# Performance work log

Measured on AMD Instinct MI355X. Metric: run time of the kernel, lower is better.

Reference implementation:

```python
import jax, jax.numpy as jnp
import numpy as np

# Topologies derived from init kwargs (inputs=64, outputs=64, state=512, net1 hidden=[512])
D = 64 + 64 + 512                      # 640 = concat(input, prev_output, state)
NET1 = [D, 512, 64]
NET3 = [D] + NET1 + [512]              # [640, 640, 512, 64, 512] (code reuses mutated net1 topo)
W_TOTAL = sum(NET3[j] * NET3[j + 1] for j in range(len(NET3) - 1))  # 802816
B_TOTAL = sum(NET3[1:])                # 1728
NET2 = [D] + NET1 + [W_TOTAL + B_TOTAL]  # [640, 640, 512, 64, 804544]


def _leaky(v):
    return jnp.where(v >= 0, v, 0.01 * v)


def setup_inputs() -> dict:
    key = jax.random.key(0)
    ks = jax.random.split(key, 16)
    inp = {
        "x": jax.random.normal(ks[0], (64,), jnp.float32),
        "prev_output": jnp.zeros((64,), jnp.float32),
        "state": jnp.zeros((512,), jnp.float32),
    }
    # net1 params (Linear stores W as [out, in])
    for i in range(len(NET1) - 1):
        inp[f"net1_w{i}"] = jax.random.normal(ks[1 + i], (NET1[i + 1], NET1[i]), jnp.float32) * 0.02
        inp[f"net1_b{i}"] = jnp.zeros((NET1[i + 1],), jnp.float32)
    # net2 params
    for i in range(len(NET2) - 1):
        inp[f"net2_w{i}"] = jax.random.normal(ks[5 + i], (NET2[i + 1], NET2[i]), jnp.float32) * 0.02
        inp[f"net2_b{i}"] = jnp.zeros((NET2[i + 1],), jnp.float32)
    return inp


def reference(x, prev_output, state,
              net1_w0, net1_b0, net1_w1, net1_b1,
              net2_w0, net2_b0, net2_w1, net2_b1,
              net2_w2, net2_b2, net2_w3, net2_b3):
    inpt = jnp.concatenate([x, prev_output, state])  # [640]

    # net2: hypernetwork producing flattened weights+biases for net3
    h = _leaky(net2_w0 @ inpt + net2_b0)
    h = _leaky(net2_w1 @ h + net2_b1)
    h = _leaky(net2_w2 @ h + net2_b2)
    x2 = jnp.tanh(net2_w3 @ h + net2_b3) * 0.5       # [W_TOTAL + B_TOTAL]
    weights = x2[:W_TOTAL]
    bias = x2[W_TOTAL:]

    # net3: apply generated weights sequentially (state update)
    x3 = inpt
    wi, bi = 0, 0
    for j in range(1, len(NET3)):
        out_d, in_d = NET3[j], NET3[j - 1]
        W = weights[wi:wi + out_d * in_d].reshape(out_d, in_d)
        b = bias[bi:bi + out_d]
        x3 = W @ x3 + b                               # 1D: x3 @ W.T == W @ x3
        if j != len(NET3) - 1:
            x3 = _leaky(x3)
        wi += out_d * in_d
        bi += out_d
    new_state = x3                                    # [512]

    # net1: output head
    h1 = _leaky(net1_w0 @ inpt + net1_b0)
    out = net1_w1 @ h1 + net1_b1                      # [64]

    # torch forward returns only `out`; new_state is the persistent buffer
    # update. We concatenate both so the full step math is observable.
    return jnp.concatenate([out, new_state])          # [576]
```

## Files before the change

### kernel.cpp

```cpp
#include <hip/hip_runtime.h>
#include <math.h>


#define WS_H0    0
#define WS_H1N1  640
#define WS_H1N2  1152
#define WS_H2    1664
#define WS_INPT  1728
#define WS_X3A   2368
#define WS_X3B   3008
#define WS_X3C   3520

__device__ __forceinline__ float leaky_f(float v) { return v >= 0.0f ? v : 0.01f * v; }

__device__ __forceinline__ float inpt_at(int i, const float* x, const float* po, const float* st) {
  return i < 64 ? x[i] : (i < 128 ? po[i - 64] : st[i - 128]);
}

__global__ __launch_bounds__(256) void k1a(const float* __restrict__ x, const float* __restrict__ po,
                                           const float* __restrict__ st,
                                           const float* __restrict__ w2_0, const float* __restrict__ b2_0,
                                           const float* __restrict__ w1_0, const float* __restrict__ b1_0,
                                           float* __restrict__ ws) {
  __shared__ float s_in[640];
  for (int i = threadIdx.x; i < 640; i += 256) {
    float v = inpt_at(i, x, po, st);
    s_in[i] = v;
    ws[WS_INPT + i] = v;
  }
  __syncthreads();
  int wave = threadIdx.x >> 6, lane = threadIdx.x & 63;
  int o = blockIdx.x * 4 + wave;
  const float* wrow;
  float bias;
  float* dst;
  if (o < 640) {
    wrow = w2_0 + (long long)o * 640; bias = b2_0[o]; dst = ws + WS_H0 + o;
  } else {
    int oo = o - 640;
    wrow = w1_0 + (long long)oo * 640; bias = b1_0[oo]; dst = ws + WS_H1N1 + oo;
  }
  float acc = 0.0f;
  for (int i = lane; i < 640; i += 64) acc += wrow[i] * s_in[i];
  for (int off = 32; off; off >>= 1) acc += __shfl_xor(acc, off, 64);
  if (lane == 0) *dst = leaky_f(acc + bias);
}

__global__ __launch_bounds__(256) void k1b(const float* __restrict__ w2_1, const float* __restrict__ b2_1,
                                           const float* __restrict__ w1_1, const float* __restrict__ b1_1,
                                           float* __restrict__ ws, float* __restrict__ out) {
  __shared__ float s_h0[640];
  __shared__ float s_h1[512];
  for (int i = threadIdx.x; i < 640; i += 256) s_h0[i] = ws[WS_H0 + i];
  for (int i = threadIdx.x; i < 512; i += 256) s_h1[i] = ws[WS_H1N1 + i];
  __syncthreads();
  int wave = threadIdx.x >> 6, lane = threadIdx.x & 63;
  int o = blockIdx.x * 4 + wave;
  float acc = 0.0f;
  if (o < 512) {
    const float* wrow = w2_1 + (long long)o * 640;
    for (int i = lane; i < 640; i += 64) acc += wrow[i] * s_h0[i];
    for (int off = 32; off; off >>= 1) acc += __shfl_xor(acc, off, 64);
    if (lane == 0) ws[WS_H1N2 + o] = leaky_f(acc + b2_1[o]);
  } else {
    int oo = o - 512;
    const float* wrow = w1_1 + (long long)oo * 512;
    for (int i = lane; i < 512; i += 64) acc += wrow[i] * s_h1[i];
    for (int off = 32; off; off >>= 1) acc += __shfl_xor(acc, off, 64);
    if (lane == 0) out[oo] = acc + b1_1[oo];
  }
}

__global__ __launch_bounds__(256) void k1c(const float* __restrict__ w2_2, const float* __restrict__ b2_2,
                                           float* __restrict__ ws) {
  __shared__ float s_h[512];
  for (int i = threadIdx.x; i < 512; i += 256) s_h[i] = ws[WS_H1N2 + i];
  __syncthreads();
  int wave = threadIdx.x >> 6, lane = threadIdx.x & 63;
  int o = blockIdx.x * 4 + wave;
  const float* wrow = w2_2 + (long long)o * 512;
  float acc = 0.0f;
  for (int i = lane; i < 512; i += 64) acc += wrow[i] * s_h[i];
  for (int off = 32; off; off >>= 1) acc += __shfl_xor(acc, off, 64);
  if (lane == 0) ws[WS_H2 + o] = leaky_f(acc + b2_2[o]);
}

template <int IN_D, bool LEAKY>
__global__ __launch_bounds__(256) void k2(const float* __restrict__ w3, const float* __restrict__ b3,
                                          const float* __restrict__ h2p, const float* __restrict__ x3in,
                                          float* __restrict__ x3out, long long wi, long long brow) {
  __shared__ float s_in[IN_D];
  __shared__ float s_red[4];
  float h[64];
  const float4* h4 = (const float4*)h2p;
#pragma unroll
  for (int k = 0; k < 16; k++) {
    float4 v = h4[k];
    h[4 * k + 0] = v.x; h[4 * k + 1] = v.y; h[4 * k + 2] = v.z; h[4 * k + 3] = v.w;
  }
  for (int i = threadIdx.x; i < IN_D; i += 256) s_in[i] = x3in[i];
  __syncthreads();

  int o = blockIdx.x;
  float acc = 0.0f;
  for (int i = threadIdx.x; i < IN_D; i += 256) {
    long long r = wi + (long long)o * IN_D + i;
    const float4* row = (const float4*)(w3 + r * 64);
    float d = 0.0f;
#pragma unroll
    for (int k = 0; k < 16; k++) {
      float4 v = row[k];
      d += v.x * h[4 * k + 0] + v.y * h[4 * k + 1] + v.z * h[4 * k + 2] + v.w * h[4 * k + 3];
    }
    float x2v = 0.5f * tanhf(d + b3[r]);
    acc += x2v * s_in[i];
  }
  for (int off = 32; off; off >>= 1) acc += __shfl_xor(acc, off, 64);
  int wave = threadIdx.x >> 6, lane = threadIdx.x & 63;
  if (lane == 0) s_red[wave] = acc;
  __syncthreads();
  if (threadIdx.x == 0) {
    float tot = s_red[0] + s_red[1] + s_red[2] + s_red[3];
    long long rb = brow + o;
    const float4* row = (const float4*)(w3 + rb * 64);
    float d = 0.0f;
#pragma unroll
    for (int k = 0; k < 16; k++) {
      float4 v = row[k];
      d += v.x * h[4 * k + 0] + v.y * h[4 * k + 1] + v.z * h[4 * k + 2] + v.w * h[4 * k + 3];
    }
    float gb = 0.5f * tanhf(d + b3[rb]);
    float res = tot + gb;
    x3out[o] = LEAKY ? leaky_f(res) : res;
  }
}

__global__ __launch_bounds__(256) void k2d(const float* __restrict__ w3, const float* __restrict__ b3,
                                           const float* __restrict__ ws, float* __restrict__ out) {
  const float* h2p = ws + WS_H2;
  float h[64];
  const float4* h4 = (const float4*)h2p;
#pragma unroll
  for (int k = 0; k < 16; k++) {
    float4 v = h4[k];
    h[4 * k + 0] = v.x; h[4 * k + 1] = v.y; h[4 * k + 2] = v.z; h[4 * k + 3] = v.w;
  }
  int wave = threadIdx.x >> 6, lane = threadIdx.x & 63;
  int o = blockIdx.x * 4 + wave;
  long long r = 770048LL + (long long)o * 64 + lane;
  const float4* row = (const float4*)(w3 + r * 64);
  float d = 0.0f;
#pragma unroll
  for (int k = 0; k < 16; k++) {
    float4 v = row[k];
    d += v.x * h[4 * k + 0] + v.y * h[4 * k + 1] + v.z * h[4 * k + 2] + v.w * h[4 * k + 3];
  }
  float x2v = 0.5f * tanhf(d + b3[r]);
  float acc = x2v * ws[WS_X3C + lane];
  for (int off = 32; off; off >>= 1) acc += __shfl_xor(acc, off, 64);
  if (lane == 0) {
    long long rb = 804032LL + o;
    const float4* brow = (const float4*)(w3 + rb * 64);
    float db = 0.0f;
#pragma unroll
    for (int k = 0; k < 16; k++) {
      float4 v = brow[k];
      db += v.x * h[4 * k + 0] + v.y * h[4 * k + 1] + v.z * h[4 * k + 2] + v.w * h[4 * k + 3];
    }
    float gb = 0.5f * tanhf(db + b3[rb]);
    out[64 + o] = acc + gb;
  }
}

extern "C" void kernel_launch(void* const* d_in, const int* in_sizes, int n_in,
                              void* d_out, int out_size, void* d_ws, size_t ws_size,
                              hipStream_t stream) {
  const float* x    = (const float*)d_in[0];
  const float* po   = (const float*)d_in[1];
  const float* st   = (const float*)d_in[2];
  const float* w1_0 = (const float*)d_in[3];
  const float* b1_0 = (const float*)d_in[4];
  const float* w1_1 = (const float*)d_in[5];
  const float* b1_1 = (const float*)d_in[6];
  const float* w2_0 = (const float*)d_in[7];
  const float* b2_0 = (const float*)d_in[8];
  const float* w2_1 = (const float*)d_in[9];
  const float* b2_1 = (const float*)d_in[10];
  const float* w2_2 = (const float*)d_in[11];
  const float* b2_2 = (const float*)d_in[12];
  const float* w3   = (const float*)d_in[13];
  const float* b3   = (const float*)d_in[14];
  float* ws  = (float*)d_ws;
  float* out = (float*)d_out;

  k1a<<<288, 256, 0, stream>>>(x, po, st, w2_0, b2_0, w1_0, b1_0, ws);
  k1b<<<144, 256, 0, stream>>>(w2_1, b2_1, w1_1, b1_1, ws, out);
  k1c<<<16, 256, 0, stream>>>(w2_2, b2_2, ws);
  k2<640, true><<<640, 256, 0, stream>>>(w3, b3, ws + WS_H2, ws + WS_INPT, ws + WS_X3A, 0LL, 802816LL);
  k2<640, true><<<512, 256, 0, stream>>>(w3, b3, ws + WS_H2, ws + WS_X3A, ws + WS_X3B, 409600LL, 803456LL);
  k2<512, true><<<64, 256, 0, stream>>>(w3, b3, ws + WS_H2, ws + WS_X3B, ws + WS_X3C, 737280LL, 803968LL);
  k2d<<<128, 256, 0, stream>>>(w3, b3, ws, out);
}
```

Before: 354.8 us.

## Vectorize dot products, uniform hidden vector, fast tanh, and 512-thread blocks for generator

Several changes land together. The net1/net2 row dot products now use float4 loads from global and shared memory. The generator kernels read the 64-element hidden vector through readfirstlane so it can live in scalar registers, and compute tanh with exp2 and a hardware reciprocal instead of tanhf. The generated-bias row is folded into the per-thread work rather than computed serially by thread 0. The k2 launches also move to 512 threads per block. The intent is to cut VGPR pressure and transcendental cost in a memory-bound kernel. The fast tanh approximation may change accuracy slightly, and with 512 threads a block for the 640-input layers has only 128 threads doing a second iteration, so load imbalance grows.

```diff
diff --git a/kernel.cpp b/kernel.cpp
--- a/kernel.cpp
+++ b/kernel.cpp
@@ -13,8 +13,55 @@
 
 __device__ __forceinline__ float leaky_f(float v) { return v >= 0.0f ? v : 0.01f * v; }
 
+__device__ __forceinline__ float uni(float v) {
+  return __int_as_float(__builtin_amdgcn_readfirstlane(__float_as_int(v)));
+}
+
 __device__ __forceinline__ float inpt_at(int i, const float* x, const float* po, const float* st) {
   return i < 64 ? x[i] : (i < 128 ? po[i - 64] : st[i - 128]);
+}
+
+__device__ __forceinline__ float x2val(const float* __restrict__ w3, const float* __restrict__ b3,
+                                       long long r, const float* hs) {
+  const float4* row = (const float4*)(w3 + (r << 6));
+  float d0 = 0.f, d1 = 0.f, d2 = 0.f, d3 = 0.f;
+#pragma unroll
+  for (int k = 0; k < 16; k++) {
+    float4 v = row[k];
+    d0 = fmaf(v.x, hs[4 * k + 0], d0);
+    d1 = fmaf(v.y, hs[4 * k + 1], d1);
+    d2 = fmaf(v.z, hs[4 * k + 2], d2);
+    d3 = fmaf(v.w, hs[4 * k + 3], d3);
+  }
+  float d = ((d0 + d1) + (d2 + d3)) + b3[r];
+  float t = exp2f(d * 2.8853900817779268f);
+  return 0.5f - __builtin_amdgcn_rcpf(t + 1.0f);
+}
+
+__device__ __forceinline__ void load_h_uniform(const float* __restrict__ h2p, float* hs) {
+  const float4* h4 = (const float4*)h2p;
+#pragma unroll
+  for (int k = 0; k < 16; k++) {
+    float4 v = h4[k];
+    hs[4 * k + 0] = uni(v.x);
+    hs[4 * k + 1] = uni(v.y);
+    hs[4 * k + 2] = uni(v.z);
+    hs[4 * k + 3] = uni(v.w);
+  }
+}
+
+template <int IN>
+__device__ __forceinline__ float row_dot(const float* __restrict__ wrow, const float* s_in, int lane) {
+  const float4* w4 = (const float4*)wrow;
+  const float4* s4 = (const float4*)s_in;
+  float acc = 0.f;
+  for (int j = lane; j < IN / 4; j += 64) {
+    float4 a = w4[j];
+    float4 b = s4[j];
+    acc += a.x * b.x + a.y * b.y + a.z * b.z + a.w * b.w;
+  }
+  for (int off = 32; off; off >>= 1) acc += __shfl_xor(acc, off, 64);
+  return acc;
 }
 
 __global__ __launch_bounds__(256) void k1a(const float* __restrict__ x, const float* __restrict__ po,
@@ -22,7 +69,7 @@
                                            const float* __restrict__ w2_0, const float* __restrict__ b2_0,
                                            const float* __restrict__ w1_0, const float* __restrict__ b1_0,
                                            float* __restrict__ ws) {
-  __shared__ float s_in[640];
+  __shared__ __align__(16) float s_in[640];
   for (int i = threadIdx.x; i < 640; i += 256) {
     float v = inpt_at(i, x, po, st);
     s_in[i] = v;
@@ -40,136 +87,83 @@
     int oo = o - 640;
     wrow = w1_0 + (long long)oo * 640; bias = b1_0[oo]; dst = ws + WS_H1N1 + oo;
   }
-  float acc = 0.0f;
-  for (int i = lane; i < 640; i += 64) acc += wrow[i] * s_in[i];
-  for (int off = 32; off; off >>= 1) acc += __shfl_xor(acc, off, 64);
+  float acc = row_dot<640>(wrow, s_in, lane);
   if (lane == 0) *dst = leaky_f(acc + bias);
 }
 
 __global__ __launch_bounds__(256) void k1b(const float* __restrict__ w2_1, const float* __restrict__ b2_1,
                                            const float* __restrict__ w1_1, const float* __restrict__ b1_1,
                                            float* __restrict__ ws, float* __restrict__ out) {
-  __shared__ float s_h0[640];
-  __shared__ float s_h1[512];
+  __shared__ __align__(16) float s_h0[640];
+  __shared__ __align__(16) float s_h1[512];
   for (int i = threadIdx.x; i < 640; i += 256) s_h0[i] = ws[WS_H0 + i];
   for (int i = threadIdx.x; i < 512; i += 256) s_h1[i] = ws[WS_H1N1 + i];
   __syncthreads();
   int wave = threadIdx.x >> 6, lane = threadIdx.x & 63;
   int o = blockIdx.x * 4 + wave;
-  float acc = 0.0f;
   if (o < 512) {
-    const float* wrow = w2_1 + (long long)o * 640;
-    for (int i = lane; i < 640; i += 64) acc += wrow[i] * s_h0[i];
-    for (int off = 32; off; off >>= 1) acc += __shfl_xor(acc, off, 64);
+    float acc = row_dot<640>(w2_1 + (long long)o * 640, s_h0, lane);
     if (lane == 0) ws[WS_H1N2 + o] = leaky_f(acc + b2_1[o]);
   } else {
     int oo = o - 512;
-    const float* wrow = w1_1 + (long long)oo * 512;
-    for (int i = lane; i < 512; i += 64) acc += wrow[i] * s_h1[i];
-    for (int off = 32; off; off >>= 1) acc += __shfl_xor(acc, off, 64);
+    float acc = row_dot<512>(w1_1 + (long long)oo * 512, s_h1, lane);
     if (lane == 0) out[oo] = acc + b1_1[oo];
   }
 }
 
 __global__ __launch_bounds__(256) void k1c(const float* __restrict__ w2_2, const float* __restrict__ b2_2,
                                            float* __restrict__ ws) {
-  __shared__ float s_h[512];
+  __shared__ __align__(16) float s_h[512];
   for (int i = threadIdx.x; i < 512; i += 256) s_h[i] = ws[WS_H1N2 + i];
   __syncthreads();
   int wave = threadIdx.x >> 6, lane = threadIdx.x & 63;
   int o = blockIdx.x * 4 + wave;
-  const float* wrow = w2_2 + (long long)o * 512;
-  float acc = 0.0f;
-  for (int i = lane; i < 512; i += 64) acc += wrow[i] * s_h[i];
-  for (int off = 32; off; off >>= 1) acc += __shfl_xor(acc, off, 64);
+  float acc = row_dot<512>(w2_2 + (long long)o * 512, s_h, lane);
   if (lane == 0) ws[WS_H2 + o] = leaky_f(acc + b2_2[o]);
 }
 
 template <int IN_D, bool LEAKY>
-__global__ __launch_bounds__(256) void k2(const float* __restrict__ w3, const float* __restrict__ b3,
+__global__ __launch_bounds__(512) void k2(const float* __restrict__ w3, const float* __restrict__ b3,
                                           const float* __restrict__ h2p, const float* __restrict__ x3in,
                                           float* __restrict__ x3out, long long wi, long long brow) {
-  __shared__ float s_in[IN_D];
-  __shared__ float s_red[4];
-  float h[64];
-  const float4* h4 = (const float4*)h2p;
-#pragma unroll
-  for (int k = 0; k < 16; k++) {
-    float4 v = h4[k];
-    h[4 * k + 0] = v.x; h[4 * k + 1] = v.y; h[4 * k + 2] = v.z; h[4 * k + 3] = v.w;
-  }
-  for (int i = threadIdx.x; i < IN_D; i += 256) s_in[i] = x3in[i];
+  __shared__ __align__(16) float s_in[IN_D];
+  __shared__ float s_red[8];
+  float hs[64];
+  load_h_uniform(h2p, hs);
+  for (int i = threadIdx.x; i < IN_D; i += 512) s_in[i] = x3in[i];
   __syncthreads();
 
   int o = blockIdx.x;
   float acc = 0.0f;
-  for (int i = threadIdx.x; i < IN_D; i += 256) {
+  for (int i = threadIdx.x; i < IN_D; i += 512) {
     long long r = wi + (long long)o * IN_D + i;
-    const float4* row = (const float4*)(w3 + r * 64);
-    float d = 0.0f;
-#pragma unroll
-    for (int k = 0; k < 16; k++) {
-      float4 v = row[k];
-      d += v.x * h[4 * k + 0] + v.y * h[4 * k + 1] + v.z * h[4 * k + 2] + v.w * h[4 * k + 3];
-    }
-    float x2v = 0.5f * tanhf(d + b3[r]);
-    acc += x2v * s_in[i];
+    acc += x2val(w3, b3, r, hs) * s_in[i];
   }
+  if (threadIdx.x == 511) acc += x2val(w3, b3, brow + o, hs);
+
   for (int off = 32; off; off >>= 1) acc += __shfl_xor(acc, off, 64);
   int wave = threadIdx.x >> 6, lane = threadIdx.x & 63;
   if (lane == 0) s_red[wave] = acc;
   __syncthreads();
   if (threadIdx.x == 0) {
-    float tot = s_red[0] + s_red[1] + s_red[2] + s_red[3];
-    long long rb = brow + o;
-    const float4* row = (const float4*)(w3 + rb * 64);
-    float d = 0.0f;
+    float tot = 0.f;
 #pragma unroll
-    for (int k = 0; k < 16; k++) {
-      float4 v = row[k];
-      d += v.x * h[4 * k + 0] + v.y * h[4 * k + 1] + v.z * h[4 * k + 2] + v.w * h[4 * k + 3];
-    }
-    float gb = 0.5f * tanhf(d + b3[rb]);
-    float res = tot + gb;
-    x3out[o] = LEAKY ? leaky_f(res) : res;
+    for (int w = 0; w < 8; w++) tot += s_red[w];
+    x3out[o] = LEAKY ? leaky_f(tot) : tot;
   }
 }
 
 __global__ __launch_bounds__(256) void k2d(const float* __restrict__ w3, const float* __restrict__ b3,
                                            const float* __restrict__ ws, float* __restrict__ out) {
-  const float* h2p = ws + WS_H2;
-  float h[64];
-  const float4* h4 = (const float4*)h2p;
-#pragma unroll
-  for (int k = 0; k < 16; k++) {
-    float4 v = h4[k];
-    h[4 * k + 0] = v.x; h[4 * k + 1] = v.y; h[4 * k + 2] = v.z; h[4 * k + 3] = v.w;
-  }
+  float hs[64];
+  load_h_uniform(ws + WS_H2, hs);
   int wave = threadIdx.x >> 6, lane = threadIdx.x & 63;
   int o = blockIdx.x * 4 + wave;
   long long r = 770048LL + (long long)o * 64 + lane;
-  const float4* row = (const float4*)(w3 + r * 64);
-  float d = 0.0f;
-#pragma unroll
-  for (int k = 0; k < 16; k++) {
-    float4 v = row[k];
-    d += v.x * h[4 * k + 0] + v.y * h[4 * k + 1] + v.z * h[4 * k + 2] + v.w * h[4 * k + 3];
-  }
-  float x2v = 0.5f * tanhf(d + b3[r]);
-  float acc = x2v * ws[WS_X3C + lane];
+  float acc = x2val(w3, b3, r, hs) * ws[WS_X3C + lane];
+  if (lane == 0) acc += x2val(w3, b3, 804032LL + o, hs);
   for (int off = 32; off; off >>= 1) acc += __shfl_xor(acc, off, 64);
-  if (lane == 0) {
-    long long rb = 804032LL + o;
-    const float4* brow = (const float4*)(w3 + rb * 64);
-    float db = 0.0f;
-#pragma unroll
-    for (int k = 0; k < 16; k++) {
-      float4 v = brow[k];
-      db += v.x * h[4 * k + 0] + v.y * h[4 * k + 1] + v.z * h[4 * k + 2] + v.w * h[4 * k + 3];
-    }
-    float gb = 0.5f * tanhf(db + b3[rb]);
-    out[64 + o] = acc + gb;
-  }
+  if (lane == 0) out[64 + o] = acc;
 }
 
 extern "C" void kernel_launch(void* const* d_in, const int* in_sizes, int n_in,
@@ -196,8 +190,8 @@
   k1a<<<288, 256, 0, stream>>>(x, po, st, w2_0, b2_0, w1_0, b1_0, ws);
   k1b<<<144, 256, 0, stream>>>(w2_1, b2_1, w1_1, b1_1, ws, out);
   k1c<<<16, 256, 0, stream>>>(w2_2, b2_2, ws);
-  k2<640, true><<<640, 256, 0, stream>>>(w3, b3, ws + WS_H2, ws + WS_INPT, ws + WS_X3A, 0LL, 802816LL);
-  k2<640, true><<<512, 256, 0, stream>>>(w3, b3, ws + WS_H2, ws + WS_X3A, ws + WS_X3B, 409600LL, 803456LL);
-  k2<512, true><<<64, 256, 0, stream>>>(w3, b3, ws + WS_H2, ws + WS_X3B, ws + WS_X3C, 737280LL, 803968LL);
+  k2<640, true><<<640, 512, 0, stream>>>(w3, b3, ws + WS_H2, ws + WS_INPT, ws + WS_X3A, 0LL, 802816LL);
+  k2<640, true><<<512, 512, 0, stream>>>(w3, b3, ws + WS_H2, ws + WS_X3A, ws + WS_X3B, 409600LL, 803456LL);
+  k2<512, true><<<64, 512, 0, stream>>>(w3, b3, ws + WS_H2, ws + WS_X3B, ws + WS_X3C, 737280LL, 803968LL);
   k2d<<<128, 256, 0, stream>>>(w3, b3, ws, out);
 }
```

Result: no change. 351.3 us (-1.0%).
